# Kernel optimization log

Hardware: AMD Instinct MI355X
Metric: run time of the kernel (lower is better)

## Reference

```python
import jax, jax.numpy as jnp
import numpy as np

LOC = 200 * 200 + 1   # location vocab
E = 100               # loc_emb_size
H = 100               # hidden_neurons (== input size of STLSTM)
D = 12                # temporal/spatial slot embedding dim
NSLOT = 92


def setup_inputs() -> dict:
    key = jax.random.key(0)
    ks = jax.random.split(key, 24)
    B, T = 1024, 256
    inp = {}
    inp["traj"] = jax.random.randint(ks[0], (B, T), 0, LOC)
    inp["lennew"] = jax.random.randint(ks[1], (B, T), 0, T)
    inp["traj_len"] = 255  # static scalar (loop runs traj_len+1 steps)
    inp["tu"] = jax.random.randint(ks[2], (B, T), 0, NSLOT)
    inp["tl"] = jax.random.randint(ks[3], (B, T), 0, NSLOT)
    inp["tu_slot"] = jax.random.randint(ks[4], (B, T), 0, NSLOT)
    inp["tl_slot"] = jax.random.randint(ks[5], (B, T), 0, NSLOT)
    inp["su"] = jax.random.randint(ks[6], (B, T), 0, NSLOT)
    inp["sl"] = jax.random.randint(ks[7], (B, T), 0, NSLOT)
    inp["su_slot"] = jax.random.randint(ks[8], (B, T), 0, NSLOT)
    inp["sl_slot"] = jax.random.randint(ks[9], (B, T), 0, NSLOT)
    # learned parameters
    inp["emb_loc"] = jax.random.normal(ks[10], (LOC, E), jnp.float32) * 0.02
    inp["emb_t"] = jax.random.normal(ks[11], (NSLOT, D), jnp.float32) * 0.02
    inp["emb_s"] = jax.random.normal(ks[12], (NSLOT, D), jnp.float32) * 0.02
    inp["W_ih"] = jax.random.normal(ks[13], (E, 4 * H), jnp.float32) * 0.05
    inp["W_hh"] = jax.random.normal(ks[14], (H, 4 * H), jnp.float32) * 0.05
    inp["b"] = jnp.zeros((4 * H,), jnp.float32)
    inp["W_xt"] = jax.random.normal(ks[15], (E, H), jnp.float32) * 0.05
    inp["W_tt"] = jax.random.normal(ks[16], (D, H), jnp.float32) * 0.05
    inp["b_t"] = jnp.zeros((H,), jnp.float32)
    inp["W_xs"] = jax.random.normal(ks[17], (E, H), jnp.float32) * 0.05
    inp["W_ss"] = jax.random.normal(ks[18], (D, H), jnp.float32) * 0.05
    inp["b_s"] = jnp.zeros((H,), jnp.float32)
    return inp


def reference(traj, lennew, traj_len, tu, tl, tu_slot, tl_slot, su, sl,
              su_slot, sl_slot, emb_loc, emb_t, emb_s, W_ih, W_hh, b,
              W_xt, W_tt, b_t, W_xs, W_ss, b_s):
    steps = int(traj_len) + 1  # static python int -> static slice
    x = emb_loc[traj[:, :steps]]            # [B, S, E] (dropout is identity in eval)
    dtype = x.dtype

    def interp(up_e, low_e, up_d, low_d):
        # linear interpolation between upper/lower slot embeddings
        up = up_d[:, :steps].astype(dtype)[..., None]
        low = low_d[:, :steps].astype(dtype)[..., None]
        return (up * low_e + low * up_e) / jnp.maximum(up + low, 1.0)

    Tq = interp(emb_t[tu[:, :steps]], emb_t[tl[:, :steps]], tu_slot, tl_slot)  # [B,S,D]
    Sq = interp(emb_s[su[:, :steps]], emb_s[sl[:, :steps]], su_slot, sl_slot)  # [B,S,D]

    B = traj.shape[0]
    h0 = jnp.zeros((B, H), dtype)
    c0 = jnp.zeros((B, H), dtype)
    xs = (x.swapaxes(0, 1), Tq.swapaxes(0, 1), Sq.swapaxes(0, 1))  # time-major

    def step(carry, inp):
        h, c = carry
        xt, tg, sg = inp
        gates = xt @ W_ih + h @ W_hh + b           # [B, 4H]
        i, f, g, o = jnp.split(gates, 4, axis=-1)
        i = jax.nn.sigmoid(i)
        f = jax.nn.sigmoid(f)
        g = jnp.tanh(g)
        o = jax.nn.sigmoid(o)
        tgate = jax.nn.sigmoid(xt @ W_xt + tg @ W_tt + b_t)  # temporal gate
        sgate = jax.nn.sigmoid(xt @ W_xs + sg @ W_ss + b_s)  # spatial gate
        c = f * c + i * tgate * sgate * g
        h = o * jnp.tanh(c)
        return (h, c), None

    (h, c), _ = jax.lax.scan(step, (h0, c0), xs)
    # model returns h at index traj_len, which is the final hidden state
    return h
```

## Files before the change

kernel.cpp:

```cpp
#include <hip/hip_runtime.h>

#define B_    1024
#define T_    256
#define LOCN  40001
#define E_    100
#define H_    100
#define NC    600

typedef float f32x2 __attribute__((ext_vector_type(2)));

__device__ __forceinline__ float fsig(float x) {
    const float e = __builtin_amdgcn_exp2f(x * -1.442695040888963f);
    return __builtin_amdgcn_rcpf(1.f + e);
}

constexpr int PROWS = 16;
constexpr int PPAD  = 20;

__global__ __launch_bounds__(320) void proj_loc_kernel(
    const float* __restrict__ emb_loc,
    const float* __restrict__ W_ih,
    const float* __restrict__ W_xt,
    const float* __restrict__ W_xs,
    const float* __restrict__ b,
    const float* __restrict__ b_t,
    const float* __restrict__ b_s,
    float* __restrict__ P)
{
    __shared__ __attribute__((aligned(16))) float aT[E_][PPAD];
    const int tid  = threadIdx.x;
    const int row0 = blockIdx.x * PROWS;

    for (int i = tid; i < PROWS * E_; i += 320) {
        int r = i / E_, k = i - r * E_;
        int rr = row0 + r;
        float v = 0.f;
        if (rr < LOCN) v = emb_loc[rr * E_ + k];
        aT[k][r] = v;
    }
    __syncthreads();
    if (tid >= 300) return;

    for (int cc = 0; cc < 2; ++cc) {
        const int c = tid + cc * 300;
        const float* wp; int stride; float bias;
        if (c < 400)      { wp = W_ih + c;         stride = 400; bias = b[c]; }
        else if (c < 500) { wp = W_xt + (c - 400); stride = 100; bias = b_t[c - 400]; }
        else              { wp = W_xs + (c - 500); stride = 100; bias = b_s[c - 500]; }

        float acc[PROWS];
        #pragma unroll
        for (int r = 0; r < PROWS; ++r) acc[r] = bias;

        for (int k = 0; k < E_; ++k) {
            float w = wp[(size_t)k * stride];
            #pragma unroll
            for (int r = 0; r < PROWS; ++r) acc[r] += aT[k][r] * w;
        }
        #pragma unroll
        for (int r = 0; r < PROWS; ++r) {
            int rr = row0 + r;
            if (rr < LOCN) P[(size_t)rr * NC + c] = acc[r];
        }
    }
}

__global__ void proj_ts_kernel(
    const float* __restrict__ emb_t, const float* __restrict__ emb_s,
    const float* __restrict__ W_tt,  const float* __restrict__ W_ss,
    float* __restrict__ P_t, float* __restrict__ P_s)
{
    int idx = blockIdx.x * 256 + threadIdx.x;
    if (idx >= 2 * 92 * H_) return;
    int which = idx / (92 * H_);
    int rem   = idx - which * (92 * H_);
    int r = rem / H_, c = rem - r * H_;
    const float* e = which ? emb_s : emb_t;
    const float* W = which ? W_ss : W_tt;
    float acc = 0.f;
    #pragma unroll
    for (int k = 0; k < 12; ++k) acc += e[r * 12 + k] * W[k * H_ + c];
    (which ? P_s : P_t)[rem] = acc;
}

constexpr int RB = 4;
constexpr int NT = 704;

__global__ __launch_bounds__(NT, 3) void lstm_rec_kernel(
    const int* __restrict__ traj,
    const int* __restrict__ traj_len_p,
    const int* __restrict__ tu,      const int* __restrict__ tl,
    const int* __restrict__ tu_slot, const int* __restrict__ tl_slot,
    const int* __restrict__ su,      const int* __restrict__ sl,
    const int* __restrict__ su_slot, const int* __restrict__ sl_slot,
    const float* __restrict__ P,
    const float* __restrict__ P_t,
    const float* __restrict__ P_s,
    const float* __restrict__ W_hh,
    float* __restrict__ out)
{
    __shared__ __attribute__((aligned(16))) float h_lds[RB][H_];
    __shared__ float gates_lds[RB][400];
    __shared__ float tg_lds[RB][H_];
    __shared__ float sg_lds[RB][H_];
    __shared__ int   loc_lds[2][RB];

    const int tid = threadIdx.x;
    const int b0  = blockIdx.x * RB;
    int steps = traj_len_p[0] + 1;
    if (steps > T_) steps = T_;

    f32x2 w2[50];
    if (tid < 400) {
        #pragma unroll
        for (int j = 0; j < 50; ++j) {
            w2[j].x = W_hh[(2 * j)     * 400 + tid];
            w2[j].y = W_hh[(2 * j + 1) * 400 + tid];
        }
        ((float*)h_lds)[tid] = 0.f;
    }
    if (tid < RB) loc_lds[0][tid] = traj[(b0 + tid) * T_];

    const int er = tid / 100;
    const int eh = tid - er * 100;
    float c_reg = 0.f, hval = 0.f;
    __syncthreads();

    for (int t = 0; t < steps; ++t) {
        const int buf = t & 1;

        if (tid >= 700) {
            int r = tid - 700;
            if (t + 1 < steps) loc_lds[buf ^ 1][r] = traj[(b0 + r) * T_ + t + 1];
        }

        if (tid < 400) {
            const int n = tid;
            float gacc[RB];
            #pragma unroll
            for (int r = 0; r < RB; ++r) {
                const int loc = __builtin_amdgcn_readfirstlane(loc_lds[buf][r]);
                const float* __restrict__ Prow = P + (size_t)loc * NC;
                gacc[r] = Prow[n];
            }

            f32x2 acc2[RB];
            #pragma unroll
            for (int r = 0; r < RB; ++r) acc2[r] = (f32x2){0.f, 0.f};
            #pragma unroll
            for (int k4 = 0; k4 < H_ / 4; ++k4) {
                #pragma unroll
                for (int r = 0; r < RB; ++r) {
                    const float4 hv = *(const float4*)(&h_lds[r][k4 * 4]);
                    const f32x2 hlo = {hv.x, hv.y};
                    const f32x2 hhi = {hv.z, hv.w};
                    acc2[r] = hlo * w2[2 * k4]     + acc2[r];
                    acc2[r] = hhi * w2[2 * k4 + 1] + acc2[r];
                }
            }
            const bool isg = (n >= 200 && n < 300);
            #pragma unroll
            for (int r = 0; r < RB; ++r) {
                float v  = (acc2[r].x + acc2[r].y) + gacc[r];
                float xx = isg ? 2.f * v : v;
                float s  = fsig(xx);
                gates_lds[r][n] = isg ? (2.f * s - 1.f) : s;
            }
        }

        if (tid >= 448 && tid < 648) {
            const int  ch   = tid - 448;
            const bool is_t = ch < 100;
            const int  hx   = is_t ? ch : ch - 100;
            const int* up_a = is_t ? tu_slot : su_slot;
            const int* lo_a = is_t ? tl_slot : sl_slot;
            const int* ui_a = is_t ? tu : su;
            const int* li_a = is_t ? tl : sl;
            const float* Pq = is_t ? P_t : P_s;
            float* dst      = is_t ? &tg_lds[0][0] : &sg_lds[0][0];
            #pragma unroll
            for (int r = 0; r < RB; ++r) {
                const int off = __builtin_amdgcn_readfirstlane((b0 + r) * T_ + t);
                const int loc = __builtin_amdgcn_readfirstlane(loc_lds[buf][r]);
                const float* __restrict__ Prow = P + (size_t)loc * NC;
                float gp  = Prow[400 + ch];
                float up  = (float)up_a[off];
                float low = (float)lo_a[off];
                int   ui  = ui_a[off], li = li_a[off];
                const float inv = __builtin_amdgcn_rcpf(fmaxf(up + low, 1.f));
                float iv  = (up * Pq[li * H_ + hx] + low * Pq[ui * H_ + hx]) * inv;
                float pre = gp + iv;
                dst[r * H_ + hx] = fsig(pre);
            }
        }
        __syncthreads();

        if (tid < 400) {
            float i_g = gates_lds[er][eh];
            float f_g = gates_lds[er][100 + eh];
            float g_g = gates_lds[er][200 + eh];
            float o_g = gates_lds[er][300 + eh];
            float tsg = tg_lds[er][eh] * sg_lds[er][eh];
            c_reg = f_g * c_reg + i_g * tsg * g_g;
            hval  = o_g * (2.f * fsig(2.f * c_reg) - 1.f);
            h_lds[er][eh] = hval;
        }
        __syncthreads();
    }

    if (tid < 400) out[b0 * H_ + tid] = hval;
}

extern "C" void kernel_launch(void* const* d_in, const int* in_sizes, int n_in,
                              void* d_out, int out_size, void* d_ws, size_t ws_size,
                              hipStream_t stream) {
    const int*   traj     = (const int*)  d_in[0];
    const int*   traj_len = (const int*)  d_in[2];
    const int*   tu       = (const int*)  d_in[3];
    const int*   tl       = (const int*)  d_in[4];
    const int*   tu_slot  = (const int*)  d_in[5];
    const int*   tl_slot  = (const int*)  d_in[6];
    const int*   su       = (const int*)  d_in[7];
    const int*   sl       = (const int*)  d_in[8];
    const int*   su_slot  = (const int*)  d_in[9];
    const int*   sl_slot  = (const int*)  d_in[10];
    const float* emb_loc  = (const float*)d_in[11];
    const float* emb_t    = (const float*)d_in[12];
    const float* emb_s    = (const float*)d_in[13];
    const float* W_ih     = (const float*)d_in[14];
    const float* W_hh     = (const float*)d_in[15];
    const float* b        = (const float*)d_in[16];
    const float* W_xt     = (const float*)d_in[17];
    const float* W_tt     = (const float*)d_in[18];
    const float* b_t      = (const float*)d_in[19];
    const float* W_xs     = (const float*)d_in[20];
    const float* W_ss     = (const float*)d_in[21];
    const float* b_s      = (const float*)d_in[22];

    float* P   = (float*)d_ws;
    float* P_t = P + (size_t)LOCN * NC;
    float* P_s = P_t + 92 * H_;

    proj_loc_kernel<<<(LOCN + PROWS - 1) / PROWS, 320, 0, stream>>>(
        emb_loc, W_ih, W_xt, W_xs, b, b_t, b_s, P);
    proj_ts_kernel<<<(2 * 92 * H_ + 255) / 256, 256, 0, stream>>>(
        emb_t, emb_s, W_tt, W_ss, P_t, P_s);
    lstm_rec_kernel<<<B_ / RB, NT, 0, stream>>>(
        traj, traj_len, tu, tl, tu_slot, tl_slot, su, sl, su_slot, sl_slot,
        P, P_t, P_s, W_hh, (float*)d_out);
}
```

Baseline: 786.2 us.

## Split W_hh recurrent dot product across thread pairs with shuffle reduction

Each of the 400 gate threads now handles two output columns over half the hidden dimension (52 padded entries), with h_lds padded to 104 floats. Partial sums are combined across the lane pair with a shuffle. Each thread's LDS reads of h are halved and every h value loaded feeds two columns, which shortens the serial dependency chain per step. The cost is extra shuffles and padded zero weights.

Result: slower. 862.2 us (+9.7%).

```diff
diff --git a/kernel.cpp b/kernel.cpp
--- a/kernel.cpp
+++ b/kernel.cpp
@@ -85,6 +85,7 @@
 
 constexpr int RB = 4;
 constexpr int NT = 704;
+constexpr int HP = 104;
 
 __global__ __launch_bounds__(NT, 3) void lstm_rec_kernel(
     const int* __restrict__ traj,
@@ -99,7 +100,7 @@
     const float* __restrict__ W_hh,
     float* __restrict__ out)
 {
-    __shared__ __attribute__((aligned(16))) float h_lds[RB][H_];
+    __shared__ __attribute__((aligned(16))) float h_lds[RB][HP];
     __shared__ float gates_lds[RB][400];
     __shared__ float tg_lds[RB][H_];
     __shared__ float sg_lds[RB][H_];
@@ -110,16 +111,27 @@
     int steps = traj_len_p[0] + 1;
     if (steps > T_) steps = T_;
 
-    f32x2 w2[50];
+    const int p     = tid >> 1;
+    const int half  = tid & 1;
+    const int kbase = half * 52;
+    const int c0    = 2 * p;
+    const int c1    = c0 + 1;
+
+    for (int i = tid; i < RB * HP; i += NT) ((float*)h_lds)[i] = 0.f;
+    if (tid < RB) loc_lds[0][tid] = traj[(b0 + tid) * T_];
+
+    f32x2 w0[26], w1[26];
     if (tid < 400) {
         #pragma unroll
-        for (int j = 0; j < 50; ++j) {
-            w2[j].x = W_hh[(2 * j)     * 400 + tid];
-            w2[j].y = W_hh[(2 * j + 1) * 400 + tid];
-        }
-        ((float*)h_lds)[tid] = 0.f;
-    }
-    if (tid < RB) loc_lds[0][tid] = traj[(b0 + tid) * T_];
+        for (int m = 0; m < 26; ++m) {
+            const int ka = kbase + 2 * m;
+            const int kb = ka + 1;
+            w0[m].x = (ka < 100) ? W_hh[ka * 400 + c0] : 0.f;
+            w0[m].y = (kb < 100) ? W_hh[kb * 400 + c0] : 0.f;
+            w1[m].x = (ka < 100) ? W_hh[ka * 400 + c1] : 0.f;
+            w1[m].y = (kb < 100) ? W_hh[kb * 400 + c1] : 0.f;
+        }
+    }
 
     const int er = tid / 100;
     const int eh = tid - er * 100;
@@ -144,24 +156,31 @@
                 gacc[r] = Prow[n];
             }
 
-            f32x2 acc2[RB];
-            #pragma unroll
-            for (int r = 0; r < RB; ++r) acc2[r] = (f32x2){0.f, 0.f};
-            #pragma unroll
-            for (int k4 = 0; k4 < H_ / 4; ++k4) {
+            f32x2 a0[RB], a1[RB];
+            #pragma unroll
+            for (int r = 0; r < RB; ++r) { a0[r] = (f32x2){0.f, 0.f}; a1[r] = (f32x2){0.f, 0.f}; }
+            #pragma unroll
+            for (int j4 = 0; j4 < 13; ++j4) {
                 #pragma unroll
                 for (int r = 0; r < RB; ++r) {
-                    const float4 hv = *(const float4*)(&h_lds[r][k4 * 4]);
+                    const float4 hv = *(const float4*)(&h_lds[r][kbase + j4 * 4]);
                     const f32x2 hlo = {hv.x, hv.y};
                     const f32x2 hhi = {hv.z, hv.w};
-                    acc2[r] = hlo * w2[2 * k4]     + acc2[r];
-                    acc2[r] = hhi * w2[2 * k4 + 1] + acc2[r];
+                    a0[r] = hlo * w0[2 * j4]     + a0[r];
+                    a0[r] = hhi * w0[2 * j4 + 1] + a0[r];
+                    a1[r] = hlo * w1[2 * j4]     + a1[r];
+                    a1[r] = hhi * w1[2 * j4 + 1] + a1[r];
                 }
             }
             const bool isg = (n >= 200 && n < 300);
             #pragma unroll
             for (int r = 0; r < RB; ++r) {
-                float v  = (acc2[r].x + acc2[r].y) + gacc[r];
+                const float s0 = a0[r].x + a0[r].y;
+                const float s1 = a1[r].x + a1[r].y;
+                const float f0 = s0 + __shfl_xor(s0, 1);
+                const float f1 = s1 + __shfl_xor(s1, 1);
+                const float sum = half ? f1 : f0;
+                float v  = sum + gacc[r];
                 float xx = isg ? 2.f * v : v;
                 float s  = fsig(xx);
                 gates_lds[r][n] = isg ? (2.f * s - 1.f) : s;
```

## Prefetch next-step projection rows and stage slot tables in LDS

Applied to the files above, without the earlier changes.

Uses a three-deep ring of location indices so each step loads the next step's gate and temporal/spatial projection rows from global memory while it computes the current step. This takes the dependent global gather latency off the serial recurrence path. It also copies P_t/P_s and all per-row slot indices and weights into LDS up front, so the interpolation reads LDS instead of global memory. The cost is a much larger shared-memory footprint (over 100 KB at RB=4), which may lower occupancy, plus extra registers for the prefetched values.

New measurement: 1.229 ms. +56.3%, slower.

```diff
diff --git a/kernel.cpp b/kernel.cpp
--- a/kernel.cpp
+++ b/kernel.cpp
@@ -103,13 +103,30 @@
     __shared__ float gates_lds[RB][400];
     __shared__ float tg_lds[RB][H_];
     __shared__ float sg_lds[RB][H_];
-    __shared__ int   loc_lds[2][RB];
+    __shared__ int   loc_lds[3][RB];
+    __shared__ float ts_f[RB][4][T_];
+    __shared__ int   ts_i[RB][4][T_];
+    __shared__ float Pt_lds[92 * H_];
+    __shared__ float Ps_lds[92 * H_];
 
     const int tid = threadIdx.x;
     const int b0  = blockIdx.x * RB;
     int steps = traj_len_p[0] + 1;
     if (steps > T_) steps = T_;
 
+    for (int i = tid; i < 92 * H_; i += NT) { Pt_lds[i] = P_t[i]; Ps_lds[i] = P_s[i]; }
+    for (int i = tid; i < RB * 4 * T_; i += NT) {
+        const int r   = i / (4 * T_);
+        const int rem = i - r * (4 * T_);
+        const int a   = rem / T_;
+        const int t   = rem - a * T_;
+        const int off = (b0 + r) * T_ + t;
+        const int* fs = (a == 0) ? tu_slot : (a == 1) ? tl_slot : (a == 2) ? su_slot : sl_slot;
+        const int* is = (a == 0) ? tu      : (a == 1) ? tl      : (a == 2) ? su      : sl;
+        ts_f[r][a][t] = (float)fs[off];
+        ts_i[r][a][t] = is[off];
+    }
+
     f32x2 w2[50];
     if (tid < 400) {
         #pragma unroll
@@ -119,31 +136,59 @@
         }
         ((float*)h_lds)[tid] = 0.f;
     }
-    if (tid < RB) loc_lds[0][tid] = traj[(b0 + tid) * T_];
+    if (tid < RB) {
+        loc_lds[0][tid] = traj[(b0 + tid) * T_];
+        loc_lds[1][tid] = traj[(b0 + tid) * T_ + ((steps > 1) ? 1 : 0)];
+    }
+
+    const bool isTS = (tid >= 448 && tid < 648);
+    const int  ch   = tid - 448;
+    const bool is_t = ch < 100;
+    const int  hx   = is_t ? ch : ch - 100;
+    const int  fa   = is_t ? 0 : 2;
+    const float* Pq = is_t ? Pt_lds : Ps_lds;
+    const int  gcol = (is_t ? 400 : 500) + hx;
+    float* dst      = is_t ? &tg_lds[0][0] : &sg_lds[0][0];
 
     const int er = tid / 100;
     const int eh = tid - er * 100;
+
+    float gacc_cur[RB];
+    if (tid < 400) {
+        #pragma unroll
+        for (int r = 0; r < RB; ++r) {
+            const int loc0 = __builtin_amdgcn_readfirstlane(traj[(b0 + r) * T_]);
+            gacc_cur[r] = P[(size_t)loc0 * NC + tid];
+        }
+    }
+    float gp_cur[RB];
+    if (isTS) {
+        #pragma unroll
+        for (int r = 0; r < RB; ++r) {
+            const int loc0 = __builtin_amdgcn_readfirstlane(traj[(b0 + r) * T_]);
+            gp_cur[r] = P[(size_t)loc0 * NC + gcol];
+        }
+    }
+
     float c_reg = 0.f, hval = 0.f;
+    int i0 = 0, i1 = 1, i2 = 2;
     __syncthreads();
 
     for (int t = 0; t < steps; ++t) {
-        const int buf = t & 1;
-
         if (tid >= 700) {
-            int r = tid - 700;
-            if (t + 1 < steps) loc_lds[buf ^ 1][r] = traj[(b0 + r) * T_ + t + 1];
+            const int r  = tid - 700;
+            const int t2 = (t + 2 < steps) ? t + 2 : steps - 1;
+            loc_lds[i2][r] = traj[(b0 + r) * T_ + t2];
         }
 
         if (tid < 400) {
             const int n = tid;
-            float gacc[RB];
-            #pragma unroll
-            for (int r = 0; r < RB; ++r) {
-                const int loc = __builtin_amdgcn_readfirstlane(loc_lds[buf][r]);
-                const float* __restrict__ Prow = P + (size_t)loc * NC;
-                gacc[r] = Prow[n];
-            }
-
+            float gacc_nxt[RB];
+            #pragma unroll
+            for (int r = 0; r < RB; ++r) {
+                const int locN = __builtin_amdgcn_readfirstlane(loc_lds[i1][r]);
+                gacc_nxt[r] = P[(size_t)locN * NC + n];
+            }
             f32x2 acc2[RB];
             #pragma unroll
             for (int r = 0; r < RB; ++r) acc2[r] = (f32x2){0.f, 0.f};
@@ -161,36 +206,30 @@
             const bool isg = (n >= 200 && n < 300);
             #pragma unroll
             for (int r = 0; r < RB; ++r) {
-                float v  = (acc2[r].x + acc2[r].y) + gacc[r];
+                float v  = (acc2[r].x + acc2[r].y) + gacc_cur[r];
                 float xx = isg ? 2.f * v : v;
                 float s  = fsig(xx);
                 gates_lds[r][n] = isg ? (2.f * s - 1.f) : s;
             }
-        }
-
-        if (tid >= 448 && tid < 648) {
-            const int  ch   = tid - 448;
-            const bool is_t = ch < 100;
-            const int  hx   = is_t ? ch : ch - 100;
-            const int* up_a = is_t ? tu_slot : su_slot;
-            const int* lo_a = is_t ? tl_slot : sl_slot;
-            const int* ui_a = is_t ? tu : su;
-            const int* li_a = is_t ? tl : sl;
-            const float* Pq = is_t ? P_t : P_s;
-            float* dst      = is_t ? &tg_lds[0][0] : &sg_lds[0][0];
-            #pragma unroll
-            for (int r = 0; r < RB; ++r) {
-                const int off = __builtin_amdgcn_readfirstlane((b0 + r) * T_ + t);
-                const int loc = __builtin_amdgcn_readfirstlane(loc_lds[buf][r]);
-                const float* __restrict__ Prow = P + (size_t)loc * NC;
-                float gp  = Prow[400 + ch];
-                float up  = (float)up_a[off];
-                float low = (float)lo_a[off];
-                int   ui  = ui_a[off], li = li_a[off];
-                const float inv = __builtin_amdgcn_rcpf(fmaxf(up + low, 1.f));
-                float iv  = (up * Pq[li * H_ + hx] + low * Pq[ui * H_ + hx]) * inv;
-                float pre = gp + iv;
-                dst[r * H_ + hx] = fsig(pre);
+            #pragma unroll
+            for (int r = 0; r < RB; ++r) gacc_cur[r] = gacc_nxt[r];
+        }
+
+        if (isTS) {
+            #pragma unroll
+            for (int r = 0; r < RB; ++r) {
+                const float up = ts_f[r][fa][t];
+                const float lo = ts_f[r][fa + 1][t];
+                const int   ui = ts_i[r][fa][t];
+                const int   li = ts_i[r][fa + 1][t];
+                const float inv = __builtin_amdgcn_rcpf(fmaxf(up + lo, 1.f));
+                const float iv  = (up * Pq[li * H_ + hx] + lo * Pq[ui * H_ + hx]) * inv;
+                dst[r * H_ + hx] = fsig(gp_cur[r] + iv);
+            }
+            #pragma unroll
+            for (int r = 0; r < RB; ++r) {
+                const int locN = __builtin_amdgcn_readfirstlane(loc_lds[i1][r]);
+                gp_cur[r] = P[(size_t)locN * NC + gcol];
             }
         }
         __syncthreads();
@@ -206,6 +245,8 @@
             h_lds[er][eh] = hval;
         }
         __syncthreads();
+
+        const int tmp = i0; i0 = i1; i1 = i2; i2 = tmp;
     }
 
     if (tid < 400) out[b0 * H_ + tid] = hval;
```
